# Optimization experiments

Measured on AMD Instinct MI355X. Metric: run time of the kernel, lower is better.

## Reference

```python
import jax, jax.numpy as jnp
import numpy as np

N_GRAPHS = 8192
NODES_PER_GRAPH = 62
IN_CH = 4
HID = 64
NUM_CLASSES = 3
DEG = 8
N = N_GRAPHS * NODES_PER_GRAPH        # 507904 total nodes
E = N * DEG                            # 4063232 edges
BN_EPS = 1e-5


def setup_inputs() -> dict:
    key = jax.random.key(0)
    ks = jax.random.split(key, 24)

    def lin_w(k, i, o):
        return (jax.random.normal(k, (i, o), jnp.float32) / np.float32(np.sqrt(i)))

    inp = {
        "x": jax.random.normal(ks[0], (N, IN_CH), jnp.float32),
        "edge_src": jax.random.randint(ks[1], (E,), 0, N, dtype=jnp.int32),
        "edge_dst": jax.random.randint(ks[2], (E,), 0, N, dtype=jnp.int32),
        "num_graphs": N_GRAPHS,
        # conv1 MLP: Linear(4,64) -> ReLU -> Linear(64,64)
        "W1a": lin_w(ks[3], IN_CH, HID), "b1a": jnp.zeros((HID,), jnp.float32),
        "W1b": lin_w(ks[4], HID, HID),   "b1b": jnp.zeros((HID,), jnp.float32),
        "g1": jnp.ones((HID,), jnp.float32), "be1": jnp.zeros((HID,), jnp.float32),
        # conv2 MLP
        "W2a": lin_w(ks[5], HID, HID), "b2a": jnp.zeros((HID,), jnp.float32),
        "W2b": lin_w(ks[6], HID, HID), "b2b": jnp.zeros((HID,), jnp.float32),
        "g2": jnp.ones((HID,), jnp.float32), "be2": jnp.zeros((HID,), jnp.float32),
        # conv3 MLP
        "W3a": lin_w(ks[7], HID, HID), "b3a": jnp.zeros((HID,), jnp.float32),
        "W3b": lin_w(ks[8], HID, HID), "b3b": jnp.zeros((HID,), jnp.float32),
        "g3": jnp.ones((HID,), jnp.float32), "be3": jnp.zeros((HID,), jnp.float32),
        # final classifier fc2 (fc1 is unused in the original forward)
        "Wfc": lin_w(ks[9], HID, NUM_CLASSES), "bfc": jnp.zeros((NUM_CLASSES,), jnp.float32),
    }
    return inp


def _gin_conv(x, src, dst, Wa, ba, Wb, bb):
    # GINConv with eps=0: mlp(x_i + sum_{j->i} x_j)
    agg = jax.ops.segment_sum(x[src], dst, num_segments=N)
    h = x + agg
    return jnp.maximum(h @ Wa + ba, 0.0) @ Wb + bb


def _bn(h, g, b):
    # BatchNorm1d with batch statistics (training-mode math)
    m = h.mean(axis=0)
    v = h.var(axis=0)
    return (h - m) * jax.lax.rsqrt(v + BN_EPS) * g + b


def reference(x, edge_src, edge_dst, num_graphs,
              W1a, b1a, W1b, b1b, g1, be1,
              W2a, b2a, W2b, b2b, g2, be2,
              W3a, b3a, W3b, b3b, g3, be3,
              Wfc, bfc):
    h = _bn(jnp.maximum(_gin_conv(x, edge_src, edge_dst, W1a, b1a, W1b, b1b), 0.0), g1, be1)
    h = _bn(jnp.maximum(_gin_conv(h, edge_src, edge_dst, W2a, b2a, W2b, b2b), 0.0), g2, be2)
    h = _bn(jnp.maximum(_gin_conv(h, edge_src, edge_dst, W3a, b3a, W3b, b3b), 0.0), g3, be3)
    h = h.reshape(num_graphs, -1, HID).sum(axis=1)   # sum-pool nodes per graph
    # dropout is identity in eval mode
    return h @ Wfc + bfc
```

## Files before the change

### kernel.cpp

```cpp
#include <hip/hip_runtime.h>
#include <hip/hip_bf16.h>

#define NN   507904
#define NE   4063232
#define NG   8192
#define NPG  62
#define NBLKM 992

#define NB    248
#define BRNG  2048
#define BCAP  17152
#define PBCAP 31744
#define P3BLK 992
#define CSRSZ (NB * PBCAP)

#define OFF_R     0
#define OFF_AGGBF (OFF_R + NN * 64)
#define OFF_CSR   (OFF_AGGBF + NN * 32)
#define OFF_OC    (OFF_CSR + CSRSZ)
#define OFF_BCUR  (OFF_OC + 2 * NN)
#define OFF_PART  (OFF_BCUR + 256)
#define OFF_WTB   (OFF_PART + NBLKM * 128)
#define OFF_SS    (OFF_WTB + 11264)

#define WB_W1B 0
#define WB_W2A 4096
#define WB_W2B 8192
#define WB_W3A 12288
#define WB_W3B 16384
#define WB_W1A 20480

typedef __attribute__((ext_vector_type(8))) short short8;
typedef __attribute__((ext_vector_type(4))) float f32x4;
typedef unsigned short ushort_t;

__device__ __forceinline__ ushort_t f2bf_bits(float f) {
  union { float f; unsigned u; } x; x.f = f;
  unsigned r = x.u + 0x7FFF + ((x.u >> 16) & 1);
  return (ushort_t)(r >> 16);
}
__device__ __forceinline__ float bf_lo(unsigned u) {
  union { unsigned i; float f; } x; x.i = u << 16; return x.f;
}
__device__ __forceinline__ float bf_hi(unsigned u) {
  union { unsigned i; float f; } x; x.i = u & 0xFFFF0000u; return x.f;
}
__device__ __forceinline__ float bf_sh(unsigned u) {
  union { unsigned i; float f; } x; x.i = u << 16; return x.f;
}

__global__ __launch_bounds__(256) void prep_weights(
    const float* __restrict__ w1a, const float* __restrict__ w1b,
    const float* __restrict__ w2a, const float* __restrict__ w2b,
    const float* __restrict__ w3a, const float* __restrict__ w3b,
    ushort_t* __restrict__ wtb, int* __restrict__ bcur,
    unsigned* __restrict__ sentinel) {
  int b = blockIdx.x, tid = threadIdx.x;
  if (b == 0) {
    ushort_t* d = wtb + WB_W1A;
    for (int i = tid; i < 2048; i += 256) {
      int n = i >> 5, k = i & 31;
      d[i] = (k < 4) ? f2bf_bits(w1a[k * 64 + n]) : (ushort_t)0;
    }
  } else if (b == 6) {
    bcur[tid] = 0;
    if (tid < 32) sentinel[tid] = 0;
  } else {
    const float* s; ushort_t* d;
    switch (b) {
      case 1: s = w1b; d = wtb + WB_W1B; break;
      case 2: s = w2a; d = wtb + WB_W2A; break;
      case 3: s = w2b; d = wtb + WB_W2B; break;
      case 4: s = w3a; d = wtb + WB_W3A; break;
      default: s = w3b; d = wtb + WB_W3B; break;
    }
    for (int i = tid; i < 4096; i += 256) {
      int k = i >> 6, n = i & 63;
      d[n * 64 + k] = f2bf_bits(s[i]);
    }
  }
}

__global__ __launch_bounds__(256) void p3_bin(
    const int* __restrict__ src, const int* __restrict__ dst,
    int* __restrict__ bcur, uint2* __restrict__ recs) {
  __shared__ int histo[256];
  __shared__ int scan_s[256];
  __shared__ int base_s[256];
  __shared__ int cur_s[256];
  __shared__ uint2 buf[4096];
  const int tid = threadIdx.x;
  const int e0 = blockIdx.x * 4096;

  histo[tid] = 0;
  __syncthreads();

  int d_[16], s_[16];
#pragma unroll
  for (int k = 0; k < 16; ++k) {
    int e = e0 + k * 256 + tid;
    d_[k] = dst[e]; s_[k] = src[e];
    atomicAdd(&histo[d_[k] >> 11], 1);
  }
  __syncthreads();

  int v = histo[tid];
  scan_s[tid] = v; __syncthreads();
  for (int s = 1; s < 256; s <<= 1) {
    int add = (tid >= s) ? scan_s[tid - s] : 0;
    __syncthreads();
    scan_s[tid] += add;
    __syncthreads();
  }
  int excl = scan_s[tid] - v;
  if (tid < NB) base_s[tid] = atomicAdd(&bcur[tid], v);
  cur_s[tid] = excl;
  histo[tid] = excl;
  __syncthreads();

#pragma unroll
  for (int k = 0; k < 16; ++k) {
    int b = d_[k] >> 11;
    int p = atomicAdd(&cur_s[b], 1);
    uint2 r; r.x = (unsigned)d_[k]; r.y = (unsigned)s_[k];
    buf[p] = r;
  }
  __syncthreads();

  for (int i = tid; i < 4096; i += 256) {
    uint2 r = buf[i];
    int b = (int)(r.x >> 11);
    int g = base_s[b] + (i - histo[b]);
    if (g < BCAP) recs[(size_t)b * BCAP + g] = r;
  }
}

__global__ __launch_bounds__(1024) void p4_build(
    const uint2* __restrict__ recs, const int* __restrict__ bcur,
    int* __restrict__ csr, int2* __restrict__ oc) {
  __shared__ int lcnt[2048];
  __shared__ int pscan[1024];
  __shared__ int sstart[2048];
  __shared__ int scur[2048];
  const int b = blockIdx.x, tid = threadIdx.x;
  int m = bcur[b]; if (m > BCAP) m = BCAP;
  const int cbase = b * PBCAP;
  const int nbase = b << 11;
  const uint2* rp = recs + (size_t)b * BCAP;

  lcnt[tid] = 0; lcnt[1024 + tid] = 0;
  __syncthreads();
  for (int i = tid; i < m; i += 1024)
    atomicAdd(&lcnt[rp[i].x & (BRNG - 1)], 1);
  __syncthreads();

  int a0 = lcnt[2 * tid], a1 = lcnt[2 * tid + 1];
  int p0 = (a0 + 7) & ~7, p1 = (a1 + 7) & ~7;
  int ps = p0 + p1;
  pscan[tid] = ps; __syncthreads();
  for (int s = 1; s < 1024; s <<= 1) {
    int add = (tid >= s) ? pscan[tid - s] : 0;
    __syncthreads();
    pscan[tid] += add;
    __syncthreads();
  }
  int e0 = pscan[tid] - ps;
  sstart[2 * tid] = e0;          scur[2 * tid] = e0;
  sstart[2 * tid + 1] = e0 + p0; scur[2 * tid + 1] = e0 + p0;
  __syncthreads();

  {
    int2 r0; r0.x = cbase + sstart[tid];        r0.y = lcnt[tid];
    int2 r1; r1.x = cbase + sstart[1024 + tid]; r1.y = lcnt[1024 + tid];
    oc[nbase + tid] = r0;
    oc[nbase + 1024 + tid] = r1;
  }
  __syncthreads();

  for (int i = tid; i < m; i += 1024) {
    uint2 r = rp[i];
    int p = atomicAdd(&scur[r.x & (BRNG - 1)], 1);
    csr[cbase + p] = (int)r.y;
  }
  __syncthreads();

#pragma unroll
  for (int k = 0; k < 2; ++k) {
    int i = k * 1024 + tid;
    int st = sstart[i], d = lcnt[i], p = (d + 7) & ~7;
    for (int q = d; q < p; ++q) csr[cbase + st + q] = NN;
  }
}

__global__ __launch_bounds__(256) void gather1(
    const float4* __restrict__ x, const int* __restrict__ csr,
    const int2* __restrict__ oc, float4* __restrict__ tout) {
  int n = blockIdx.x * 256 + threadIdx.x;
  float4 a = x[n];
  int2 oc_ = oc[n];
  int off = oc_.x, deg = oc_.y;
  const int* cp = csr + off;
  int j = 0;
  for (; j + 4 <= deg; j += 4) {
    int s0 = cp[j], s1 = cp[j + 1], s2 = cp[j + 2], s3 = cp[j + 3];
    float4 v0 = x[s0], v1 = x[s1], v2 = x[s2], v3 = x[s3];
    a.x += v0.x + v1.x + v2.x + v3.x;
    a.y += v0.y + v1.y + v2.y + v3.y;
    a.z += v0.z + v1.z + v2.z + v3.z;
    a.w += v0.w + v1.w + v2.w + v3.w;
  }
  for (; j < deg; ++j) {
    float4 v = x[cp[j]];
    a.x += v.x; a.y += v.y; a.z += v.z; a.w += v.w;
  }
  tout[n] = a;
}

__global__ __launch_bounds__(256) void gather64v5(
    const ushort_t* __restrict__ h, const int* __restrict__ csr,
    const int2* __restrict__ oc, const float* __restrict__ ss,
    ushort_t* __restrict__ tout) {
  const int lane = threadIdx.x & 63;
  const int n0 = blockIdx.x * 16 + ((threadIdx.x >> 6) << 2);

  int2 ocv[4];
#pragma unroll
  for (int p = 0; p < 4; ++p) ocv[p] = oc[n0 + p];
  const float sc = ss[lane];
  const float sf = ss[64 + lane];

  float acc[4];
#pragma unroll
  for (int p = 0; p < 4; ++p)
    acc[p] = bf_sh(h[(unsigned)(n0 + p) * 64u + lane]);

  int ch[4];
#pragma unroll
  for (int p = 0; p < 4; ++p) ch[p] = (ocv[p].y + 7) >> 3;
  int cm = ch[0] > ch[1] ? ch[0] : ch[1];
  cm = cm > ch[2] ? cm : ch[2];
  cm = cm > ch[3] ? cm : ch[3];

  for (int c = 0; c < cm; ++c) {
    int4 ia[4], ib[4];
#pragma unroll
    for (int p = 0; p < 4; ++p) {
      if (c < ch[p]) {
        const int* cp = csr + ocv[p].x + (c << 3);
        ia[p] = *(const int4*)cp;
        ib[p] = *(const int4*)(cp + 4);
      } else {
        ia[p] = (int4){NN, NN, NN, NN};
        ib[p] = (int4){NN, NN, NN, NN};
      }
    }
    unsigned v[32];
#pragma unroll
    for (int p = 0; p < 4; ++p) {
      v[p * 8 + 0] = h[(unsigned)ia[p].x * 64u + lane];
      v[p * 8 + 1] = h[(unsigned)ia[p].y * 64u + lane];
      v[p * 8 + 2] = h[(unsigned)ia[p].z * 64u + lane];
      v[p * 8 + 3] = h[(unsigned)ia[p].w * 64u + lane];
      v[p * 8 + 4] = h[(unsigned)ib[p].x * 64u + lane];
      v[p * 8 + 5] = h[(unsigned)ib[p].y * 64u + lane];
      v[p * 8 + 6] = h[(unsigned)ib[p].z * 64u + lane];
      v[p * 8 + 7] = h[(unsigned)ib[p].w * 64u + lane];
    }
#pragma unroll
    for (int p = 0; p < 4; ++p) {
      acc[p] += ((bf_sh(v[p * 8 + 0]) + bf_sh(v[p * 8 + 1])) +
                 (bf_sh(v[p * 8 + 2]) + bf_sh(v[p * 8 + 3]))) +
                ((bf_sh(v[p * 8 + 4]) + bf_sh(v[p * 8 + 5])) +
                 (bf_sh(v[p * 8 + 6]) + bf_sh(v[p * 8 + 7])));
    }
  }

#pragma unroll
  for (int p = 0; p < 4; ++p) {
    const float m1 = (float)(ocv[p].y + 1);
    tout[(unsigned)(n0 + p) * 64u + lane] = f2bf_bits(fmaf(sc, acc[p], m1 * sf));
  }
}

template <bool L1, bool BFOUT>
__global__ __launch_bounds__(256) void mlp_mfma(
    const void* __restrict__ tin,
    const ushort_t* __restrict__ WaTb,
    const float* __restrict__ ba,
    const ushort_t* __restrict__ WbTb,
    const float* __restrict__ bb,
    float* __restrict__ routf, ushort_t* __restrict__ routb,
    float* __restrict__ part) {
  __shared__ __align__(16) ushort_t zt[4096];
  __shared__ float red[512];
  const int tid = threadIdx.x;
  const int wave = tid >> 6, lane = tid & 63;
  const int col = lane & 15, quad = lane >> 4;

  short8 bWa1[4];
  short8 bWa[2][4];
  short8 bWb[2][4];
#pragma unroll
  for (int nt = 0; nt < 4; ++nt) {
    if (L1) {
      bWa1[nt] = *(const short8*)(WaTb + (nt * 16 + col) * 32 + quad * 8);
    } else {
#pragma unroll
      for (int k0 = 0; k0 < 2; ++k0)
        bWa[k0][nt] = *(const short8*)(WaTb + (nt * 16 + col) * 64 + k0 * 32 + quad * 8);
    }
#pragma unroll
    for (int k0 = 0; k0 < 2; ++k0)
      bWb[k0][nt] = *(const short8*)(WbTb + (nt * 16 + col) * 64 + k0 * 32 + quad * 8);
  }
  float ba_n[4], bb_n[4];
#pragma unroll
  for (int nt = 0; nt < 4; ++nt) {
    ba_n[nt] = ba[nt * 16 + col];
    bb_n[nt] = bb[nt * 16 + col];
  }

  const int wbase = wave * 1024;
  float scol[4] = {0, 0, 0, 0}, qcol[4] = {0, 0, 0, 0};

  for (int it = 0; it < 8; ++it) {
    const int tile = blockIdx.x * 512 + it * 64 + wave * 16;

    f32x4 acc1[4];
#pragma unroll
    for (int nt = 0; nt < 4; ++nt) acc1[nt] = (f32x4){0.f, 0.f, 0.f, 0.f};

    if constexpr (L1) {
      float4 t4 = ((const float4*)tin)[tile + col];
      short8 az = {0, 0, 0, 0, 0, 0, 0, 0};
      if (quad == 0) {
        az[0] = (short)f2bf_bits(t4.x);
        az[1] = (short)f2bf_bits(t4.y);
        az[2] = (short)f2bf_bits(t4.z);
        az[3] = (short)f2bf_bits(t4.w);
      }
#pragma unroll
      for (int nt = 0; nt < 4; ++nt)
        acc1[nt] = __builtin_amdgcn_mfma_f32_16x16x32_bf16(az, bWa1[nt], acc1[nt], 0, 0, 0);
    } else {
      const ushort_t* tb = (const ushort_t*)tin;
      short8 a0 = *(const short8*)(tb + (size_t)(tile + col) * 64 + quad * 8);
      short8 a1 = *(const short8*)(tb + (size_t)(tile + col) * 64 + 32 + quad * 8);
#pragma unroll
      for (int nt = 0; nt < 4; ++nt) {
        acc1[nt] = __builtin_amdgcn_mfma_f32_16x16x32_bf16(a0, bWa[0][nt], acc1[nt], 0, 0, 0);
        acc1[nt] = __builtin_amdgcn_mfma_f32_16x16x32_bf16(a1, bWa[1][nt], acc1[nt], 0, 0, 0);
      }
    }

#pragma unroll
    for (int nt = 0; nt < 4; ++nt) {
      int oblk = nt * 2 + (col >> 3);
#pragma unroll
      for (int r = 0; r < 4; ++r) {
        int row = quad * 4 + r;
        float z = fmaxf(acc1[nt][r] + ba_n[nt], 0.0f);
        zt[wbase + row * 64 + (((oblk ^ (row & 7)) << 3) | (col & 7))] = f2bf_bits(z);
      }
    }
    short8 az0 = *(const short8*)&zt[wbase + col * 64 + ((quad ^ (col & 7)) << 3)];
    short8 az1 = *(const short8*)&zt[wbase + col * 64 + (((4 + quad) ^ (col & 7)) << 3)];

    f32x4 acc2[4];
#pragma unroll
    for (int nt = 0; nt < 4; ++nt) acc2[nt] = (f32x4){0.f, 0.f, 0.f, 0.f};
#pragma unroll
    for (int nt = 0; nt < 4; ++nt) {
      acc2[nt] = __builtin_amdgcn_mfma_f32_16x16x32_bf16(az0, bWb[0][nt], acc2[nt], 0, 0, 0);
      acc2[nt] = __builtin_amdgcn_mfma_f32_16x16x32_bf16(az1, bWb[1][nt], acc2[nt], 0, 0, 0);
    }
#pragma unroll
    for (int nt = 0; nt < 4; ++nt) {
#pragma unroll
      for (int r = 0; r < 4; ++r) {
        int row = tile + quad * 4 + r;
        float v = fmaxf(acc2[nt][r] + bb_n[nt], 0.0f);
        if (BFOUT) routb[(size_t)row * 64 + nt * 16 + col] = f2bf_bits(v);
        else       routf[(size_t)row * 64 + nt * 16 + col] = v;
        scol[nt] += v; qcol[nt] += v * v;
      }
    }
  }

#pragma unroll
  for (int nt = 0; nt < 4; ++nt) {
    float s = scol[nt], q = qcol[nt];
    s += __shfl_xor(s, 16); s += __shfl_xor(s, 32);
    q += __shfl_xor(q, 16); q += __shfl_xor(q, 32);
    if (quad == 0) {
      red[wave * 128 + nt * 16 + col] = s;
      red[wave * 128 + 64 + nt * 16 + col] = q;
    }
  }
  __syncthreads();
  if (tid < 128)
    part[blockIdx.x * 128 + tid] =
        red[tid] + red[128 + tid] + red[256 + tid] + red[384 + tid];
}

__global__ __launch_bounds__(256) void reduce_finalize(
    const float* __restrict__ part, const float* __restrict__ gma,
    const float* __restrict__ bta, float* __restrict__ ss) {
  __shared__ double sh[512];
  const int c = blockIdx.x, tid = threadIdx.x;
  double a = 0.0, b = 0.0;
  for (int blk = tid; blk < NBLKM; blk += 256) {
    a += (double)part[blk * 128 + c];
    b += (double)part[blk * 128 + 64 + c];
  }
  sh[tid] = a; sh[256 + tid] = b;
  __syncthreads();
  for (int s = 128; s; s >>= 1) {
    if (tid < s) { sh[tid] += sh[tid + s]; sh[256 + tid] += sh[256 + tid + s]; }
    __syncthreads();
  }
  if (tid == 0) {
    double mean = sh[0] / (double)NN;
    double var = sh[256] / (double)NN - mean * mean;
    double sc = (double)gma[c] / sqrt(var + 1e-5);
    ss[c] = (float)sc;
    ss[64 + c] = (float)((double)bta[c] - mean * sc);
  }
}

__global__ __launch_bounds__(64) void pool_fc(
    const float* __restrict__ r3, const float* __restrict__ ss,
    const float* __restrict__ wfc, const float* __restrict__ bfc,
    float* __restrict__ out) {
  int g = blockIdx.x, c = threadIdx.x;
  const float* base = r3 + (size_t)g * NPG * 64;
  float s = 0.f;
#pragma unroll
  for (int n = 0; n < NPG; ++n) s += base[n * 64 + c];
  float pooled = fmaf(ss[c], s, (float)NPG * ss[64 + c]);
#pragma unroll
  for (int j = 0; j < 3; ++j) {
    float v = pooled * wfc[c * 3 + j];
    for (int m = 32; m; m >>= 1) v += __shfl_xor(v, m);
    if (c == 0) out[g * 3 + j] = v + bfc[j];
  }
}

extern "C" void kernel_launch(void* const* d_in, const int* in_sizes, int n_in,
                              void* d_out, int out_size, void* d_ws, size_t ws_size,
                              hipStream_t stream) {
  const float* x    = (const float*)d_in[0];
  const int*   srcE = (const int*)d_in[1];
  const int*   dstE = (const int*)d_in[2];
  const float* W1a = (const float*)d_in[4],  *b1a = (const float*)d_in[5];
  const float* W1b = (const float*)d_in[6],  *b1b = (const float*)d_in[7];
  const float* g1  = (const float*)d_in[8],  *be1 = (const float*)d_in[9];
  const float* W2a = (const float*)d_in[10], *b2a = (const float*)d_in[11];
  const float* W2b = (const float*)d_in[12], *b2b = (const float*)d_in[13];
  const float* g2  = (const float*)d_in[14], *be2 = (const float*)d_in[15];
  const float* W3a = (const float*)d_in[16], *b3a = (const float*)d_in[17];
  const float* W3b = (const float*)d_in[18], *b3b = (const float*)d_in[19];
  const float* g3  = (const float*)d_in[20], *be3 = (const float*)d_in[21];
  const float* Wfc = (const float*)d_in[22], *bfc = (const float*)d_in[23];

  float* ws = (float*)d_ws;
  ushort_t* Rb     = (ushort_t*)(ws + OFF_R);
  float*    Rf     = ws + OFF_R;
  void*     AGGBF  = (void*)(ws + OFF_AGGBF);
  uint2*    RECS   = (uint2*)(ws + OFF_AGGBF);
  int*      CSR    = (int*)(ws + OFF_CSR);
  int2*     OC     = (int2*)(ws + OFF_OC);
  int*      BCUR   = (int*)(ws + OFF_BCUR);
  float*    PART   = ws + OFF_PART;
  ushort_t* WTB    = (ushort_t*)(ws + OFF_WTB);
  float*    SS     = ws + OFF_SS;

  prep_weights<<<7, 256, 0, stream>>>(W1a, W1b, W2a, W2b, W3a, W3b, WTB, BCUR,
                                      (unsigned*)(Rb + (size_t)NN * 64));

  p3_bin<<<P3BLK, 256, 0, stream>>>(srcE, dstE, BCUR, RECS);
  p4_build<<<NB, 1024, 0, stream>>>(RECS, BCUR, CSR, OC);

  gather1<<<NN / 256, 256, 0, stream>>>((const float4*)x, CSR, OC,
                                        (float4*)AGGBF);
  mlp_mfma<true, true><<<NBLKM, 256, 0, stream>>>(AGGBF, WTB + WB_W1A, b1a,
                                                  WTB + WB_W1B, b1b,
                                                  nullptr, Rb, PART);
  reduce_finalize<<<64, 256, 0, stream>>>(PART, g1, be1, SS + 0);

  gather64v5<<<NN / 16, 256, 0, stream>>>(Rb, CSR, OC, SS + 0,
                                          (ushort_t*)AGGBF);
  mlp_mfma<false, true><<<NBLKM, 256, 0, stream>>>(AGGBF, WTB + WB_W2A, b2a,
                                                   WTB + WB_W2B, b2b,
                                                   nullptr, Rb, PART);
  reduce_finalize<<<64, 256, 0, stream>>>(PART, g2, be2, SS + 128);

  gather64v5<<<NN / 16, 256, 0, stream>>>(Rb, CSR, OC, SS + 128,
                                          (ushort_t*)AGGBF);
  mlp_mfma<false, false><<<NBLKM, 256, 0, stream>>>(AGGBF, WTB + WB_W3A, b3a,
                                                    WTB + WB_W3B, b3b,
                                                    Rf, nullptr, PART);
  reduce_finalize<<<64, 256, 0, stream>>>(PART, g3, be3, SS + 256);

  pool_fc<<<NG, 64, 0, stream>>>(Rf, SS + 256, Wfc, bfc, (float*)d_out);
}
```

Before: 660.3 us.

## Fuse neighbor gather and BN-affine into MLP MFMA kernel for layers 2-3

Removes the separate gather64v5 kernel and folds neighbor aggregation directly into a new mlp_fused kernel. Each lane gathers a full row segment with 16-byte vector loads and builds the MFMA A operand in registers, so the aggregated activations are no longer written to and re-read from global memory. Layer 2 now writes its output to a separate buffer so layer 3 does not overwrite the input it is still gathering from, and an extra sentinel row is zeroed. The tradeoff is that each lane now handles one node with a serial edge loop, which lowers memory-level parallelism compared with the old kernel that processed four nodes per wave with lanes spread across features. It also increases register pressure in the fused kernel.

```diff
diff --git a/kernel.cpp b/kernel.cpp
--- a/kernel.cpp
+++ b/kernel.cpp
@@ -16,7 +16,7 @@
 
 #define OFF_R     0
 #define OFF_AGGBF (OFF_R + NN * 64)
-#define OFF_CSR   (OFF_AGGBF + NN * 32)
+#define OFF_CSR   (OFF_AGGBF + NN * 32 + 32)
 #define OFF_OC    (OFF_CSR + CSRSZ)
 #define OFF_BCUR  (OFF_OC + 2 * NN)
 #define OFF_PART  (OFF_BCUR + 256)
@@ -39,14 +39,8 @@
   unsigned r = x.u + 0x7FFF + ((x.u >> 16) & 1);
   return (ushort_t)(r >> 16);
 }
-__device__ __forceinline__ float bf_lo(unsigned u) {
-  union { unsigned i; float f; } x; x.i = u << 16; return x.f;
-}
-__device__ __forceinline__ float bf_hi(unsigned u) {
-  union { unsigned i; float f; } x; x.i = u & 0xFFFF0000u; return x.f;
-}
-__device__ __forceinline__ float bf_sh(unsigned u) {
-  union { unsigned i; float f; } x; x.i = u << 16; return x.f;
+__device__ __forceinline__ float bfu(ushort_t u) {
+  union { unsigned i; float f; } x; x.i = ((unsigned)u) << 16; return x.f;
 }
 
 __global__ __launch_bounds__(256) void prep_weights(
@@ -54,7 +48,7 @@
     const float* __restrict__ w2a, const float* __restrict__ w2b,
     const float* __restrict__ w3a, const float* __restrict__ w3b,
     ushort_t* __restrict__ wtb, int* __restrict__ bcur,
-    unsigned* __restrict__ sentinel) {
+    unsigned* __restrict__ sent1, unsigned* __restrict__ sent2) {
   int b = blockIdx.x, tid = threadIdx.x;
   if (b == 0) {
     ushort_t* d = wtb + WB_W1A;
@@ -64,7 +58,7 @@
     }
   } else if (b == 6) {
     bcur[tid] = 0;
-    if (tid < 32) sentinel[tid] = 0;
+    if (tid < 32) { sent1[tid] = 0; sent2[tid] = 0; }
   } else {
     const float* s; ushort_t* d;
     switch (b) {
@@ -216,72 +210,6 @@
   tout[n] = a;
 }
 
-__global__ __launch_bounds__(256) void gather64v5(
-    const ushort_t* __restrict__ h, const int* __restrict__ csr,
-    const int2* __restrict__ oc, const float* __restrict__ ss,
-    ushort_t* __restrict__ tout) {
-  const int lane = threadIdx.x & 63;
-  const int n0 = blockIdx.x * 16 + ((threadIdx.x >> 6) << 2);
-
-  int2 ocv[4];
-#pragma unroll
-  for (int p = 0; p < 4; ++p) ocv[p] = oc[n0 + p];
-  const float sc = ss[lane];
-  const float sf = ss[64 + lane];
-
-  float acc[4];
-#pragma unroll
-  for (int p = 0; p < 4; ++p)
-    acc[p] = bf_sh(h[(unsigned)(n0 + p) * 64u + lane]);
-
-  int ch[4];
-#pragma unroll
-  for (int p = 0; p < 4; ++p) ch[p] = (ocv[p].y + 7) >> 3;
-  int cm = ch[0] > ch[1] ? ch[0] : ch[1];
-  cm = cm > ch[2] ? cm : ch[2];
-  cm = cm > ch[3] ? cm : ch[3];
-
-  for (int c = 0; c < cm; ++c) {
-    int4 ia[4], ib[4];
-#pragma unroll
-    for (int p = 0; p < 4; ++p) {
-      if (c < ch[p]) {
-        const int* cp = csr + ocv[p].x + (c << 3);
-        ia[p] = *(const int4*)cp;
-        ib[p] = *(const int4*)(cp + 4);
-      } else {
-        ia[p] = (int4){NN, NN, NN, NN};
-        ib[p] = (int4){NN, NN, NN, NN};
-      }
-    }
-    unsigned v[32];
-#pragma unroll
-    for (int p = 0; p < 4; ++p) {
-      v[p * 8 + 0] = h[(unsigned)ia[p].x * 64u + lane];
-      v[p * 8 + 1] = h[(unsigned)ia[p].y * 64u + lane];
-      v[p * 8 + 2] = h[(unsigned)ia[p].z * 64u + lane];
-      v[p * 8 + 3] = h[(unsigned)ia[p].w * 64u + lane];
-      v[p * 8 + 4] = h[(unsigned)ib[p].x * 64u + lane];
-      v[p * 8 + 5] = h[(unsigned)ib[p].y * 64u + lane];
-      v[p * 8 + 6] = h[(unsigned)ib[p].z * 64u + lane];
-      v[p * 8 + 7] = h[(unsigned)ib[p].w * 64u + lane];
-    }
-#pragma unroll
-    for (int p = 0; p < 4; ++p) {
-      acc[p] += ((bf_sh(v[p * 8 + 0]) + bf_sh(v[p * 8 + 1])) +
-                 (bf_sh(v[p * 8 + 2]) + bf_sh(v[p * 8 + 3]))) +
-                ((bf_sh(v[p * 8 + 4]) + bf_sh(v[p * 8 + 5])) +
-                 (bf_sh(v[p * 8 + 6]) + bf_sh(v[p * 8 + 7])));
-    }
-  }
-
-#pragma unroll
-  for (int p = 0; p < 4; ++p) {
-    const float m1 = (float)(ocv[p].y + 1);
-    tout[(unsigned)(n0 + p) * 64u + lane] = f2bf_bits(fmaf(sc, acc[p], m1 * sf));
-  }
-}
-
 template <bool L1, bool BFOUT>
 __global__ __launch_bounds__(256) void mlp_mfma(
     const void* __restrict__ tin,
@@ -382,6 +310,151 @@
         float v = fmaxf(acc2[nt][r] + bb_n[nt], 0.0f);
         if (BFOUT) routb[(size_t)row * 64 + nt * 16 + col] = f2bf_bits(v);
         else       routf[(size_t)row * 64 + nt * 16 + col] = v;
+        scol[nt] += v; qcol[nt] += v * v;
+      }
+    }
+  }
+
+#pragma unroll
+  for (int nt = 0; nt < 4; ++nt) {
+    float s = scol[nt], q = qcol[nt];
+    s += __shfl_xor(s, 16); s += __shfl_xor(s, 32);
+    q += __shfl_xor(q, 16); q += __shfl_xor(q, 32);
+    if (quad == 0) {
+      red[wave * 128 + nt * 16 + col] = s;
+      red[wave * 128 + 64 + nt * 16 + col] = q;
+    }
+  }
+  __syncthreads();
+  if (tid < 128)
+    part[blockIdx.x * 128 + tid] =
+        red[tid] + red[128 + tid] + red[256 + tid] + red[384 + tid];
+}
+
+template <bool BFOUT>
+__global__ __launch_bounds__(256) void mlp_fused(
+    const ushort_t* __restrict__ h,
+    const int* __restrict__ csr, const int2* __restrict__ oc,
+    const float* __restrict__ ss,
+    const ushort_t* __restrict__ WaTb,
+    const float* __restrict__ ba,
+    const ushort_t* __restrict__ WbTb,
+    const float* __restrict__ bb,
+    float* __restrict__ routf, ushort_t* __restrict__ routb,
+    float* __restrict__ part) {
+  __shared__ __align__(16) ushort_t zt[4096];
+  __shared__ float red[512];
+  __shared__ float ssl[128];
+  const int tid = threadIdx.x;
+  const int wave = tid >> 6, lane = tid & 63;
+  const int col = lane & 15, quad = lane >> 4;
+  if (tid < 128) ssl[tid] = ss[tid];
+
+  short8 bWa[2][4], bWb[2][4];
+#pragma unroll
+  for (int nt = 0; nt < 4; ++nt) {
+#pragma unroll
+    for (int k0 = 0; k0 < 2; ++k0) {
+      bWa[k0][nt] = *(const short8*)(WaTb + (nt * 16 + col) * 64 + k0 * 32 + quad * 8);
+      bWb[k0][nt] = *(const short8*)(WbTb + (nt * 16 + col) * 64 + k0 * 32 + quad * 8);
+    }
+  }
+  float ba_n[4], bb_n[4];
+#pragma unroll
+  for (int nt = 0; nt < 4; ++nt) {
+    ba_n[nt] = ba[nt * 16 + col];
+    bb_n[nt] = bb[nt * 16 + col];
+  }
+  __syncthreads();
+
+  const float* scA = ssl + quad * 8;
+  const float* scB = ssl + 32 + quad * 8;
+  const float* sfA = ssl + 64 + quad * 8;
+  const float* sfB = ssl + 96 + quad * 8;
+
+  const int wbase = wave * 1024;
+  float scol[4] = {0, 0, 0, 0}, qcol[4] = {0, 0, 0, 0};
+
+  for (int it = 0; it < 8; ++it) {
+    const int tile = blockIdx.x * 512 + it * 64 + wave * 16;
+    const int row = tile + col;
+    const int2 o = oc[row];
+
+    const ushort_t* hp = h + (size_t)(unsigned)row * 64u + quad * 8;
+    short8 sl0 = *(const short8*)hp;
+    short8 sl1 = *(const short8*)(hp + 32);
+    float accA[8], accB[8];
+#pragma unroll
+    for (int e = 0; e < 8; ++e) {
+      accA[e] = bfu((ushort_t)sl0[e]);
+      accB[e] = bfu((ushort_t)sl1[e]);
+    }
+
+    const int chunks = (o.y + 7) >> 3;
+    for (int c = 0; c < chunks; ++c) {
+      const int* cp = csr + o.x + (c << 3);
+      int4 i0 = *(const int4*)cp;
+      int4 i1 = *(const int4*)(cp + 4);
+      int idx[8] = {i0.x, i0.y, i0.z, i0.w, i1.x, i1.y, i1.z, i1.w};
+#pragma unroll
+      for (int j = 0; j < 8; ++j) {
+        const ushort_t* p = h + (size_t)(unsigned)idx[j] * 64u + quad * 8;
+        short8 l0 = *(const short8*)p;
+        short8 l1 = *(const short8*)(p + 32);
+#pragma unroll
+        for (int e = 0; e < 8; ++e) {
+          accA[e] += bfu((ushort_t)l0[e]);
+          accB[e] += bfu((ushort_t)l1[e]);
+        }
+      }
+    }
+
+    const float m1 = (float)(o.y + 1);
+    short8 a0, a1;
+#pragma unroll
+    for (int e = 0; e < 8; ++e) {
+      a0[e] = (short)f2bf_bits(fmaf(scA[e], accA[e], m1 * sfA[e]));
+      a1[e] = (short)f2bf_bits(fmaf(scB[e], accB[e], m1 * sfB[e]));
+    }
+
+    f32x4 acc1[4];
+#pragma unroll
+    for (int nt = 0; nt < 4; ++nt) acc1[nt] = (f32x4){0.f, 0.f, 0.f, 0.f};
+#pragma unroll
+    for (int nt = 0; nt < 4; ++nt) {
+      acc1[nt] = __builtin_amdgcn_mfma_f32_16x16x32_bf16(a0, bWa[0][nt], acc1[nt], 0, 0, 0);
+      acc1[nt] = __builtin_amdgcn_mfma_f32_16x16x32_bf16(a1, bWa[1][nt], acc1[nt], 0, 0, 0);
+    }
+
+#pragma unroll
+    for (int nt = 0; nt < 4; ++nt) {
+      int oblk = nt * 2 + (col >> 3);
+#pragma unroll
+      for (int r = 0; r < 4; ++r) {
+        int rw = quad * 4 + r;
+        float z = fmaxf(acc1[nt][r] + ba_n[nt], 0.0f);
+        zt[wbase + rw * 64 + (((oblk ^ (rw & 7)) << 3) | (col & 7))] = f2bf_bits(z);
+      }
+    }
+    short8 az0 = *(const short8*)&zt[wbase + col * 64 + ((quad ^ (col & 7)) << 3)];
+    short8 az1 = *(const short8*)&zt[wbase + col * 64 + (((4 + quad) ^ (col & 7)) << 3)];
+
+    f32x4 acc2[4];
+#pragma unroll
+    for (int nt = 0; nt < 4; ++nt) acc2[nt] = (f32x4){0.f, 0.f, 0.f, 0.f};
+#pragma unroll
+    for (int nt = 0; nt < 4; ++nt) {
+      acc2[nt] = __builtin_amdgcn_mfma_f32_16x16x32_bf16(az0, bWb[0][nt], acc2[nt], 0, 0, 0);
+      acc2[nt] = __builtin_amdgcn_mfma_f32_16x16x32_bf16(az1, bWb[1][nt], acc2[nt], 0, 0, 0);
+    }
+#pragma unroll
+    for (int nt = 0; nt < 4; ++nt) {
+#pragma unroll
+      for (int r = 0; r < 4; ++r) {
+        int rw = tile + quad * 4 + r;
+        float v = fmaxf(acc2[nt][r] + bb_n[nt], 0.0f);
+        if (BFOUT) routb[(size_t)rw * 64 + nt * 16 + col] = f2bf_bits(v);
+        else       routf[(size_t)rw * 64 + nt * 16 + col] = v;
         scol[nt] += v; qcol[nt] += v * v;
       }
     }
@@ -466,7 +539,8 @@
   float* ws = (float*)d_ws;
   ushort_t* Rb     = (ushort_t*)(ws + OFF_R);
   float*    Rf     = ws + OFF_R;
-  void*     AGGBF  = (void*)(ws + OFF_AGGBF);
+  ushort_t* Ab     = (ushort_t*)(ws + OFF_AGGBF);
+  void*     T1     = (void*)(ws + OFF_AGGBF);
   uint2*    RECS   = (uint2*)(ws + OFF_AGGBF);
   int*      CSR    = (int*)(ws + OFF_CSR);
   int2*     OC     = (int2*)(ws + OFF_OC);
@@ -476,30 +550,28 @@
   float*    SS     = ws + OFF_SS;
 
   prep_weights<<<7, 256, 0, stream>>>(W1a, W1b, W2a, W2b, W3a, W3b, WTB, BCUR,
-                                      (unsigned*)(Rb + (size_t)NN * 64));
+                                      (unsigned*)(Rb + (size_t)NN * 64),
+                                      (unsigned*)(Ab + (size_t)NN * 64));
 
   p3_bin<<<P3BLK, 256, 0, stream>>>(srcE, dstE, BCUR, RECS);
   p4_build<<<NB, 1024, 0, stream>>>(RECS, BCUR, CSR, OC);
 
-  gather1<<<NN / 256, 256, 0, stream>>>((const float4*)x, CSR, OC,
-                                        (float4*)AGGBF);
-  mlp_mfma<true, true><<<NBLKM, 256, 0, stream>>>(AGGBF, WTB + WB_W1A, b1a,
+  gather1<<<NN / 256, 256, 0, stream>>>((const float4*)x, CSR, OC, (float4*)T1);
+  mlp_mfma<true, true><<<NBLKM, 256, 0, stream>>>(T1, WTB + WB_W1A, b1a,
                                                   WTB + WB_W1B, b1b,
                                                   nullptr, Rb, PART);
   reduce_finalize<<<64, 256, 0, stream>>>(PART, g1, be1, SS + 0);
 
-  gather64v5<<<NN / 16, 256, 0, stream>>>(Rb, CSR, OC, SS + 0,
-                                          (ushort_t*)AGGBF);
-  mlp_mfma<false, true><<<NBLKM, 256, 0, stream>>>(AGGBF, WTB + WB_W2A, b2a,
-                                                   WTB + WB_W2B, b2b,
-                                                   nullptr, Rb, PART);
+  mlp_fused<true><<<NBLKM, 256, 0, stream>>>(Rb, CSR, OC, SS + 0,
+                                             WTB + WB_W2A, b2a,
+                                             WTB + WB_W2B, b2b,
+                                             nullptr, Ab, PART);
   reduce_finalize<<<64, 256, 0, stream>>>(PART, g2, be2, SS + 128);
 
-  gather64v5<<<NN / 16, 256, 0, stream>>>(Rb, CSR, OC, SS + 128,
-                                          (ushort_t*)AGGBF);
-  mlp_mfma<false, false><<<NBLKM, 256, 0, stream>>>(AGGBF, WTB + WB_W3A, b3a,
-                                                    WTB + WB_W3B, b3b,
-                                                    Rf, nullptr, PART);
+  mlp_fused<false><<<NBLKM, 256, 0, stream>>>(Ab, CSR, OC, SS + 128,
+                                              WTB + WB_W3A, b3a,
+                                              WTB + WB_W3B, b3b,
+                                              Rf, nullptr, PART);
   reduce_finalize<<<64, 256, 0, stream>>>(PART, g3, be3, SS + 256);
 
   pool_fc<<<NG, 64, 0, stream>>>(Rf, SS + 256, Wfc, bfc, (float*)d_out);
```

Measured after the change: 567.8 us. 14.0% less time.
